# Kernel tuning notes

Hardware: AMD Instinct MI355X
Metric: run time of the kernel (lower is better)

Reference implementation:

```python
import jax, jax.numpy as jnp
import numpy as np

NODE_DIM = 256
EDGE_DIM = 128
HEADS = 8
HEAD_DIM = 32
HIDDEN = HEADS * HEAD_DIM  # 256
B, N = 2, 768
LN_EPS = 1e-5


def _layernorm(x, w, b):
    mu = jnp.mean(x, axis=-1, keepdims=True)
    var = jnp.mean(jnp.square(x - mu), axis=-1, keepdims=True)
    return (x - mu) * jax.lax.rsqrt(var + LN_EPS) * w + b


def setup_inputs() -> dict:
    key = jax.random.key(0)
    ks = jax.random.split(key, 10)
    s_node = NODE_DIM ** -0.5
    s_edge = EDGE_DIM ** -0.5
    s_hid = HIDDEN ** -0.5
    return {
        "node": jax.random.normal(ks[0], (B, N, NODE_DIM), jnp.float32),
        "edge": jax.random.normal(ks[1], (B, N, N, EDGE_DIM), jnp.float32),
        "ln_node_w": jnp.ones((NODE_DIM,), jnp.float32),
        "ln_node_b": jnp.zeros((NODE_DIM,), jnp.float32),
        "ln_edge_w": jnp.ones((EDGE_DIM,), jnp.float32),
        "ln_edge_b": jnp.zeros((EDGE_DIM,), jnp.float32),
        "Wq": jax.random.normal(ks[2], (NODE_DIM, HIDDEN), jnp.float32) * s_node,
        "Wk": jax.random.normal(ks[3], (NODE_DIM, HIDDEN), jnp.float32) * s_node,
        "Wv": jax.random.normal(ks[4], (NODE_DIM, HIDDEN), jnp.float32) * s_node,
        "Wb": jax.random.normal(ks[5], (EDGE_DIM, HEADS), jnp.float32) * s_edge,
        "Wg": jax.random.normal(ks[6], (NODE_DIM, HIDDEN), jnp.float32) * s_node,
        "bg": jnp.zeros((HIDDEN,), jnp.float32),
        "Wo": jax.random.normal(ks[7], (HIDDEN, NODE_DIM), jnp.float32) * s_hid,
        "bo": jnp.zeros((NODE_DIM,), jnp.float32),
    }


def reference(node, edge, ln_node_w, ln_node_b, ln_edge_w, ln_edge_b,
              Wq, Wk, Wv, Wb, Wg, bg, Wo, bo):
    scale = HEAD_DIM ** -0.5
    x = _layernorm(node, ln_node_w, ln_node_b)          # [b, i, node_dim]
    y = _layernorm(edge, ln_edge_w, ln_edge_b)          # [b, i, j, edge_dim]

    def heads(t):  # [b, i, hidden] -> [b, h, i, d]
        b_, i_, _ = t.shape
        return t.reshape(b_, i_, HEADS, HEAD_DIM).transpose(0, 2, 1, 3)

    q = heads(x @ Wq)
    k = heads(x @ Wk)
    v = heads(x @ Wv)
    g = heads(jax.nn.sigmoid(x @ Wg + bg))
    bias = jnp.einsum('bije,eh->bhij', y, Wb)           # [b, h, i, j]

    logits = jnp.einsum('bhid,bhjd->bhij', q, k) * scale + bias
    attn = jax.nn.softmax(logits, axis=-1)
    res = jnp.einsum('bhij,bhjd->bhid', attn, v) * g    # gated values
    res = res.transpose(0, 2, 1, 3).reshape(node.shape[0], node.shape[1], HIDDEN)
    return res @ Wo + bo
```

## Files before the change

### kernel.cpp

```cpp
#include <hip/hip_runtime.h>
#include <hip/hip_bf16.h>
#include <math.h>

#define BN 1536
#define NN 768
#define SCALE 0.17677669529663687f
#define NROWS (BN * NN)

__device__ __forceinline__ float sel8(const float* a, int idx) {
    float r = a[0];
#pragma unroll
    for (int t = 1; t < 8; ++t) r = (idx == t) ? a[t] : r;
    return r;
}

__global__ __launch_bounds__(256) void k_lnproj(
    const float* __restrict__ node, const float* __restrict__ lnw,
    const float* __restrict__ lnb, const float* __restrict__ Wq,
    const float* __restrict__ Wk, const float* __restrict__ Wv,
    const float* __restrict__ Wg, const float* __restrict__ bg,
    float* __restrict__ q, float* __restrict__ k,
    float* __restrict__ v, float* __restrict__ g)
{
    __shared__ float xs[8][256];
    const int tid = threadIdx.x;
    const int wave = tid >> 6, lane = tid & 63;
    const int row0 = blockIdx.x * 8;

#pragma unroll
    for (int rr = 0; rr < 2; ++rr) {
        const int r = wave * 2 + rr;
        float4 xv = ((const float4*)node)[(size_t)(row0 + r) * 64 + lane];
        float s1 = xv.x + xv.y + xv.z + xv.w;
        float s2 = fmaf(xv.x, xv.x, fmaf(xv.y, xv.y, fmaf(xv.z, xv.z, xv.w * xv.w)));
#pragma unroll
        for (int off = 32; off > 0; off >>= 1) {
            s1 += __shfl_xor(s1, off);
            s2 += __shfl_xor(s2, off);
        }
        const float mu = s1 * (1.f / 256.f);
        const float rstd = rsqrtf(s2 * (1.f / 256.f) - mu * mu + 1e-5f);
        float4 w4 = ((const float4*)lnw)[lane];
        float4 b4 = ((const float4*)lnb)[lane];
        xs[r][lane * 4 + 0] = (xv.x - mu) * rstd * w4.x + b4.x;
        xs[r][lane * 4 + 1] = (xv.y - mu) * rstd * w4.y + b4.y;
        xs[r][lane * 4 + 2] = (xv.z - mu) * rstd * w4.z + b4.z;
        xs[r][lane * 4 + 3] = (xv.w - mu) * rstd * w4.w + b4.w;
    }
    __syncthreads();

    float aq[8] = {}, ak[8] = {}, av[8] = {}, ag[8] = {};
    for (int e4 = 0; e4 < 64; ++e4) {
        const int e = e4 * 4;
        float wq_[4], wk_[4], wv_[4], wg_[4];
#pragma unroll
        for (int t = 0; t < 4; ++t) {
            wq_[t] = Wq[(e + t) * 256 + tid];
            wk_[t] = Wk[(e + t) * 256 + tid];
            wv_[t] = Wv[(e + t) * 256 + tid];
            wg_[t] = Wg[(e + t) * 256 + tid];
        }
#pragma unroll
        for (int r = 0; r < 8; ++r) {
            float4 xr = *(const float4*)&xs[r][e];
            aq[r] = fmaf(xr.x, wq_[0], fmaf(xr.y, wq_[1], fmaf(xr.z, wq_[2], fmaf(xr.w, wq_[3], aq[r]))));
            ak[r] = fmaf(xr.x, wk_[0], fmaf(xr.y, wk_[1], fmaf(xr.z, wk_[2], fmaf(xr.w, wk_[3], ak[r]))));
            av[r] = fmaf(xr.x, wv_[0], fmaf(xr.y, wv_[1], fmaf(xr.z, wv_[2], fmaf(xr.w, wv_[3], av[r]))));
            ag[r] = fmaf(xr.x, wg_[0], fmaf(xr.y, wg_[1], fmaf(xr.z, wg_[2], fmaf(xr.w, wg_[3], ag[r]))));
        }
    }
    const float bgv = bg[tid];
#pragma unroll
    for (int r = 0; r < 8; ++r) {
        const size_t o = (size_t)(row0 + r) * 256 + tid;
        q[o] = aq[r] * SCALE;
        k[o] = ak[r];
        v[o] = av[r];
        g[o] = 1.f / (1.f + __expf(-(ag[r] + bgv)));
    }
}

__global__ __launch_bounds__(256) void k_bias(
    const float* __restrict__ edge, const float* __restrict__ lnw,
    const float* __restrict__ lnb, const float* __restrict__ Wb,
    float* __restrict__ bias)
{
    const int tid = threadIdx.x;
    const int gl = tid & 15;

    float wbf[8][8];
    float c1p[8], c0p[8];
#pragma unroll
    for (int hh = 0; hh < 8; ++hh) { c1p[hh] = 0.f; c0p[hh] = 0.f; }
#pragma unroll
    for (int t = 0; t < 8; ++t) {
        const int c = gl * 8 + t;
        const float w = lnw[c], bb = lnb[c];
#pragma unroll
        for (int hh = 0; hh < 8; ++hh) {
            const float wb_ = Wb[c * 8 + hh];
            wbf[t][hh] = w * wb_;
            c1p[hh] += wbf[t][hh];
            c0p[hh] = fmaf(bb, wb_, c0p[hh]);
        }
    }
#pragma unroll
    for (int off = 1; off < 16; off <<= 1) {
#pragma unroll
        for (int hh = 0; hh < 8; ++hh) {
            c1p[hh] += __shfl_xor(c1p[hh], off);
            c0p[hh] += __shfl_xor(c0p[hh], off);
        }
    }
    const float c1s = sel8(c1p, gl & 7);
    const float c0s = sel8(c0p, gl & 7);

    const int stride = gridDim.x * 16;
    for (int r = blockIdx.x * 16 + (tid >> 4); r < NROWS; r += stride) {
        const float4 e0 = ((const float4*)edge)[(size_t)r * 32 + gl * 2];
        const float4 e1 = ((const float4*)edge)[(size_t)r * 32 + gl * 2 + 1];
        float s1 = (e0.x + e0.y) + (e0.z + e0.w) + ((e1.x + e1.y) + (e1.z + e1.w));
        float s2 = fmaf(e0.x, e0.x, fmaf(e0.y, e0.y, fmaf(e0.z, e0.z, e0.w * e0.w)));
        s2 = fmaf(e1.x, e1.x, fmaf(e1.y, e1.y, fmaf(e1.z, e1.z, fmaf(e1.w, e1.w, s2))));
        float d[8];
#pragma unroll
        for (int hh = 0; hh < 8; ++hh) {
            float t0 = e0.x * wbf[0][hh];
            t0 = fmaf(e0.y, wbf[1][hh], t0);
            t0 = fmaf(e0.z, wbf[2][hh], t0);
            t0 = fmaf(e0.w, wbf[3][hh], t0);
            t0 = fmaf(e1.x, wbf[4][hh], t0);
            t0 = fmaf(e1.y, wbf[5][hh], t0);
            t0 = fmaf(e1.z, wbf[6][hh], t0);
            t0 = fmaf(e1.w, wbf[7][hh], t0);
            d[hh] = t0;
        }
#pragma unroll
        for (int off = 1; off < 16; off <<= 1) {
            s1 += __shfl_xor(s1, off);
            s2 += __shfl_xor(s2, off);
#pragma unroll
            for (int hh = 0; hh < 8; ++hh) d[hh] += __shfl_xor(d[hh], off);
        }
        if (gl < 8) {
            const float mu = s1 * (1.f / 128.f);
            const float rstd = rsqrtf(s2 * (1.f / 128.f) - mu * mu + 1e-5f);
            const float dh = sel8(d, gl);
            bias[(size_t)r * 8 + gl] = rstd * (dh - mu * c1s) + c0s;
        }
    }
}

__global__ __launch_bounds__(256) void k_attn2(
    const float* __restrict__ bias,
    const float* __restrict__ q, const float* __restrict__ k,
    const float* __restrict__ v, const float* __restrict__ g,
    float* __restrict__ res)
{
    __shared__ float mrg[4][64][6];
    const int tid = threadIdx.x;
    const int wave = tid >> 6, lane = tid & 63;
    const int bi = blockIdx.x;
    const int b = bi / NN;
    const int h = lane >> 3;

    const float4 q4 = ((const float4*)q)[(size_t)bi * 64 + lane];
    const float* brow = bias + (size_t)bi * NN * 8;
    const size_t kb = (size_t)b * NN * 64;

    float m = -3e38f, s = 0.f;
    float4 acc = make_float4(0.f, 0.f, 0.f, 0.f);

    for (int jp = wave * 2; jp < NN; jp += 8) {
        const int j0 = jp, j1 = jp + 1;
        const float4 k0 = ((const float4*)k)[kb + (size_t)j0 * 64 + lane];
        const float4 k1 = ((const float4*)k)[kb + (size_t)j1 * 64 + lane];
        const float b0 = brow[j0 * 8 + h];
        const float b1 = brow[j1 * 8 + h];
        const float4 v0 = ((const float4*)v)[kb + (size_t)j0 * 64 + lane];
        const float4 v1 = ((const float4*)v)[kb + (size_t)j1 * 64 + lane];

        float d0 = fmaf(q4.x, k0.x, fmaf(q4.y, k0.y, fmaf(q4.z, k0.z, q4.w * k0.w)));
        float d1 = fmaf(q4.x, k1.x, fmaf(q4.y, k1.y, fmaf(q4.z, k1.z, q4.w * k1.w)));
        d0 += __shfl_xor(d0, 1); d1 += __shfl_xor(d1, 1);
        d0 += __shfl_xor(d0, 2); d1 += __shfl_xor(d1, 2);
        d0 += __shfl_xor(d0, 4); d1 += __shfl_xor(d1, 4);
        const float l0 = d0 + b0;
        const float l1 = d1 + b1;

        const float mn = fmaxf(m, fmaxf(l0, l1));
        const float sc = __expf(m - mn);
        const float p0 = __expf(l0 - mn);
        const float p1 = __expf(l1 - mn);
        s = fmaf(s, sc, p0 + p1);
        m = mn;
        acc.x = fmaf(p1, v1.x, fmaf(p0, v0.x, acc.x * sc));
        acc.y = fmaf(p1, v1.y, fmaf(p0, v0.y, acc.y * sc));
        acc.z = fmaf(p1, v1.z, fmaf(p0, v0.z, acc.z * sc));
        acc.w = fmaf(p1, v1.w, fmaf(p0, v0.w, acc.w * sc));
    }

    mrg[wave][lane][0] = m;
    mrg[wave][lane][1] = s;
    mrg[wave][lane][2] = acc.x;
    mrg[wave][lane][3] = acc.y;
    mrg[wave][lane][4] = acc.z;
    mrg[wave][lane][5] = acc.w;
    __syncthreads();
    if (wave == 0) {
        float M = mrg[0][lane][0];
#pragma unroll
        for (int w2 = 1; w2 < 4; ++w2) M = fmaxf(M, mrg[w2][lane][0]);
        float S = 0.f;
        float4 A = make_float4(0.f, 0.f, 0.f, 0.f);
#pragma unroll
        for (int w2 = 0; w2 < 4; ++w2) {
            const float sc = __expf(mrg[w2][lane][0] - M);
            S = fmaf(mrg[w2][lane][1], sc, S);
            A.x = fmaf(mrg[w2][lane][2], sc, A.x);
            A.y = fmaf(mrg[w2][lane][3], sc, A.y);
            A.z = fmaf(mrg[w2][lane][4], sc, A.z);
            A.w = fmaf(mrg[w2][lane][5], sc, A.w);
        }
        const float4 g4 = ((const float4*)g)[(size_t)bi * 64 + lane];
        const float inv = 1.f / S;
        float4 r;
        r.x = A.x * inv * g4.x;
        r.y = A.y * inv * g4.y;
        r.z = A.z * inv * g4.z;
        r.w = A.w * inv * g4.w;
        ((float4*)res)[(size_t)bi * 64 + lane] = r;
    }
}

__global__ __launch_bounds__(256) void k_outproj(
    const float* __restrict__ res, const float* __restrict__ Wo,
    const float* __restrict__ bo, float* __restrict__ out)
{
    __shared__ float xs[8][256];
    const int tid = threadIdx.x;
    const int row0 = blockIdx.x * 8;

#pragma unroll
    for (int t = tid; t < 512; t += 256)
        ((float4*)&xs[0][0])[t] = ((const float4*)(res + (size_t)row0 * 256))[t];
    __syncthreads();

    float a[8] = {};
    for (int e4 = 0; e4 < 64; ++e4) {
        const int e = e4 * 4;
        float w_[4];
#pragma unroll
        for (int t = 0; t < 4; ++t) w_[t] = Wo[(e + t) * 256 + tid];
#pragma unroll
        for (int r = 0; r < 8; ++r) {
            float4 xr = *(const float4*)&xs[r][e];
            a[r] = fmaf(xr.x, w_[0], fmaf(xr.y, w_[1], fmaf(xr.z, w_[2], fmaf(xr.w, w_[3], a[r]))));
        }
    }
    const float bov = bo[tid];
#pragma unroll
    for (int r = 0; r < 8; ++r)
        out[(size_t)(row0 + r) * 256 + tid] = a[r] + bov;
}

extern "C" void kernel_launch(void* const* d_in, const int* in_sizes, int n_in,
                              void* d_out, int out_size, void* d_ws, size_t ws_size,
                              hipStream_t stream) {
    const float* node = (const float*)d_in[0];
    const float* edge = (const float*)d_in[1];
    const float* lnnw = (const float*)d_in[2];
    const float* lnnb = (const float*)d_in[3];
    const float* lnew = (const float*)d_in[4];
    const float* lneb = (const float*)d_in[5];
    const float* Wq   = (const float*)d_in[6];
    const float* Wk   = (const float*)d_in[7];
    const float* Wv   = (const float*)d_in[8];
    const float* Wb   = (const float*)d_in[9];
    const float* Wg   = (const float*)d_in[10];
    const float* bg   = (const float*)d_in[11];
    const float* Wo   = (const float*)d_in[12];
    const float* bo   = (const float*)d_in[13];
    float* out = (float*)d_out;

    float* ws = (float*)d_ws;
    const size_t NT = (size_t)BN * 256;
    float* q    = ws;
    float* k    = ws + NT;
    float* v    = ws + 2 * NT;
    float* g    = ws + 3 * NT;
    float* res  = ws + 4 * NT;
    float* bias = ws + 5 * NT;

    k_lnproj<<<BN / 8, 256, 0, stream>>>(node, lnnw, lnnb, Wq, Wk, Wv, Wg, bg, q, k, v, g);
    k_bias<<<2048, 256, 0, stream>>>(edge, lnew, lneb, Wb, bias);
    k_attn2<<<BN, 256, 0, stream>>>(bias, q, k, v, g, res);
    k_outproj<<<BN / 8, 256, 0, stream>>>(res, Wo, bo, out);
}
```

Baseline: 405.3 us.

## Prefetch edge rows and K/V tiles, use DPP reductions, one query row per wave

The bias kernel now gives each wave a contiguous 288-row chunk, loads channel-interleaved float4s, software-prefetches the next rows, and replaces shuffle reductions with DPP row reductions. The attention kernel maps one query row per wave instead of splitting the keys across four waves, so the LDS merge and the barrier go away. It processes 4 keys per step with register double-buffered K/V and bias prefetch, using DPP for part of the dot-product reduction. The risks are fewer waves working on each row (1536 waves total), higher register pressure, and a longer serial loop per wave.

```diff
diff --git a/kernel.cpp b/kernel.cpp
--- a/kernel.cpp
+++ b/kernel.cpp
@@ -12,6 +12,27 @@
 #pragma unroll
     for (int t = 1; t < 8; ++t) r = (idx == t) ? a[t] : r;
     return r;
+}
+
+__device__ __forceinline__ float dpp_add16(float x) {
+    int t;
+    t = __builtin_amdgcn_update_dpp(0, __float_as_int(x), 0x128, 0xF, 0xF, true);
+    x += __int_as_float(t);
+    t = __builtin_amdgcn_update_dpp(0, __float_as_int(x), 0x124, 0xF, 0xF, true);
+    x += __int_as_float(t);
+    t = __builtin_amdgcn_update_dpp(0, __float_as_int(x), 0x122, 0xF, 0xF, true);
+    x += __int_as_float(t);
+    t = __builtin_amdgcn_update_dpp(0, __float_as_int(x), 0x121, 0xF, 0xF, true);
+    x += __int_as_float(t);
+    return x;
+}
+__device__ __forceinline__ float dpp_xor1_add(float x) {
+    int t = __builtin_amdgcn_update_dpp(0, __float_as_int(x), 0xB1, 0xF, 0xF, true);
+    return x + __int_as_float(t);
+}
+__device__ __forceinline__ float dpp_xor2_add(float x) {
+    int t = __builtin_amdgcn_update_dpp(0, __float_as_int(x), 0x4E, 0xF, 0xF, true);
+    return x + __int_as_float(t);
 }
 
 __global__ __launch_bounds__(256) void k_lnproj(
@@ -80,87 +101,107 @@
     }
 }
 
-__global__ __launch_bounds__(256) void k_bias(
+__global__ __launch_bounds__(256, 4) void k_bias(
     const float* __restrict__ edge, const float* __restrict__ lnw,
     const float* __restrict__ lnb, const float* __restrict__ Wb,
     float* __restrict__ bias)
 {
     const int tid = threadIdx.x;
-    const int gl = tid & 15;
+    const int wv = tid >> 6, lane = tid & 63;
+    const int gl = lane & 15;
+    const int rg = lane >> 4;
 
     float wbf[8][8];
-    float c1p[8], c0p[8];
-#pragma unroll
-    for (int hh = 0; hh < 8; ++hh) { c1p[hh] = 0.f; c0p[hh] = 0.f; }
+    float c1s[8], c0s[8];
+#pragma unroll
+    for (int hh = 0; hh < 8; ++hh) { c1s[hh] = 0.f; c0s[hh] = 0.f; }
 #pragma unroll
     for (int t = 0; t < 8; ++t) {
-        const int c = gl * 8 + t;
+        const int c = (t < 4) ? (gl * 4 + t) : (64 + gl * 4 + (t - 4));
         const float w = lnw[c], bb = lnb[c];
+        const float4 wa = ((const float4*)Wb)[c * 2];
+        const float4 wc = ((const float4*)Wb)[c * 2 + 1];
+        wbf[t][0] = w * wa.x; wbf[t][1] = w * wa.y;
+        wbf[t][2] = w * wa.z; wbf[t][3] = w * wa.w;
+        wbf[t][4] = w * wc.x; wbf[t][5] = w * wc.y;
+        wbf[t][6] = w * wc.z; wbf[t][7] = w * wc.w;
+        c0s[0] = fmaf(bb, wa.x, c0s[0]); c0s[1] = fmaf(bb, wa.y, c0s[1]);
+        c0s[2] = fmaf(bb, wa.z, c0s[2]); c0s[3] = fmaf(bb, wa.w, c0s[3]);
+        c0s[4] = fmaf(bb, wc.x, c0s[4]); c0s[5] = fmaf(bb, wc.y, c0s[5]);
+        c0s[6] = fmaf(bb, wc.z, c0s[6]); c0s[7] = fmaf(bb, wc.w, c0s[7]);
+#pragma unroll
+        for (int hh = 0; hh < 8; ++hh) c1s[hh] += wbf[t][hh];
+    }
+#pragma unroll
+    for (int hh = 0; hh < 8; ++hh) {
+        c1s[hh] = dpp_add16(c1s[hh]);
+        c0s[hh] = dpp_add16(c0s[hh]);
+    }
+    const float c1l = sel8(c1s, gl & 7);
+    const float c0l = sel8(c0s, gl & 7);
+
+    const int w = blockIdx.x * 4 + wv;
+    const int row0 = w * 288;
+    const float4* ep = (const float4*)edge;
+
+    float4 a0, a1, b0, b1;
+    {
+        const size_t r = (size_t)(row0 + rg);
+        a0 = ep[r * 32 + gl];
+        a1 = ep[r * 32 + 16 + gl];
+    }
+
+    for (int it = 0; it < 72; ++it) {
+        if (it < 71) {
+            const size_t r = (size_t)(row0 + (it + 1) * 4 + rg);
+            b0 = ep[r * 32 + gl];
+            b1 = ep[r * 32 + 16 + gl];
+        }
+
+        float s1 = ((a0.x + a0.y) + (a0.z + a0.w)) + ((a1.x + a1.y) + (a1.z + a1.w));
+        float s2 = fmaf(a0.x, a0.x, fmaf(a0.y, a0.y, fmaf(a0.z, a0.z, a0.w * a0.w)));
+        s2 = fmaf(a1.x, a1.x, fmaf(a1.y, a1.y, fmaf(a1.z, a1.z, fmaf(a1.w, a1.w, s2))));
+
+        float d[8];
 #pragma unroll
         for (int hh = 0; hh < 8; ++hh) {
-            const float wb_ = Wb[c * 8 + hh];
-            wbf[t][hh] = w * wb_;
-            c1p[hh] += wbf[t][hh];
-            c0p[hh] = fmaf(bb, wb_, c0p[hh]);
-        }
-    }
-#pragma unroll
-    for (int off = 1; off < 16; off <<= 1) {
-#pragma unroll
-        for (int hh = 0; hh < 8; ++hh) {
-            c1p[hh] += __shfl_xor(c1p[hh], off);
-            c0p[hh] += __shfl_xor(c0p[hh], off);
-        }
-    }
-    const float c1s = sel8(c1p, gl & 7);
-    const float c0s = sel8(c0p, gl & 7);
-
-    const int stride = gridDim.x * 16;
-    for (int r = blockIdx.x * 16 + (tid >> 4); r < NROWS; r += stride) {
-        const float4 e0 = ((const float4*)edge)[(size_t)r * 32 + gl * 2];
-        const float4 e1 = ((const float4*)edge)[(size_t)r * 32 + gl * 2 + 1];
-        float s1 = (e0.x + e0.y) + (e0.z + e0.w) + ((e1.x + e1.y) + (e1.z + e1.w));
-        float s2 = fmaf(e0.x, e0.x, fmaf(e0.y, e0.y, fmaf(e0.z, e0.z, e0.w * e0.w)));
-        s2 = fmaf(e1.x, e1.x, fmaf(e1.y, e1.y, fmaf(e1.z, e1.z, fmaf(e1.w, e1.w, s2))));
-        float d[8];
-#pragma unroll
-        for (int hh = 0; hh < 8; ++hh) {
-            float t0 = e0.x * wbf[0][hh];
-            t0 = fmaf(e0.y, wbf[1][hh], t0);
-            t0 = fmaf(e0.z, wbf[2][hh], t0);
-            t0 = fmaf(e0.w, wbf[3][hh], t0);
-            t0 = fmaf(e1.x, wbf[4][hh], t0);
-            t0 = fmaf(e1.y, wbf[5][hh], t0);
-            t0 = fmaf(e1.z, wbf[6][hh], t0);
-            t0 = fmaf(e1.w, wbf[7][hh], t0);
-            d[hh] = t0;
-        }
-#pragma unroll
-        for (int off = 1; off < 16; off <<= 1) {
-            s1 += __shfl_xor(s1, off);
-            s2 += __shfl_xor(s2, off);
-#pragma unroll
-            for (int hh = 0; hh < 8; ++hh) d[hh] += __shfl_xor(d[hh], off);
-        }
+            float a = a0.x * wbf[0][hh];
+            a = fmaf(a0.y, wbf[1][hh], a);
+            a = fmaf(a0.z, wbf[2][hh], a);
+            a = fmaf(a0.w, wbf[3][hh], a);
+            a = fmaf(a1.x, wbf[4][hh], a);
+            a = fmaf(a1.y, wbf[5][hh], a);
+            a = fmaf(a1.z, wbf[6][hh], a);
+            a = fmaf(a1.w, wbf[7][hh], a);
+            d[hh] = a;
+        }
+
+        s1 = dpp_add16(s1);
+        s2 = dpp_add16(s2);
+#pragma unroll
+        for (int hh = 0; hh < 8; ++hh) d[hh] = dpp_add16(d[hh]);
+
+        const float mu = s1 * (1.f / 128.f);
+        const float rstd = rsqrtf(s2 * (1.f / 128.f) - mu * mu + 1e-5f);
         if (gl < 8) {
-            const float mu = s1 * (1.f / 128.f);
-            const float rstd = rsqrtf(s2 * (1.f / 128.f) - mu * mu + 1e-5f);
             const float dh = sel8(d, gl);
-            bias[(size_t)r * 8 + gl] = rstd * (dh - mu * c1s) + c0s;
-        }
-    }
-}
-
-__global__ __launch_bounds__(256) void k_attn2(
+            bias[(size_t)(row0 + it * 4 + rg) * 8 + gl] =
+                rstd * (dh - mu * c1l) + c0l;
+        }
+
+        a0 = b0; a1 = b1;
+    }
+}
+
+__global__ __launch_bounds__(256) void k_attn4(
     const float* __restrict__ bias,
     const float* __restrict__ q, const float* __restrict__ k,
     const float* __restrict__ v, const float* __restrict__ g,
     float* __restrict__ res)
 {
-    __shared__ float mrg[4][64][6];
     const int tid = threadIdx.x;
-    const int wave = tid >> 6, lane = tid & 63;
-    const int bi = blockIdx.x;
+    const int wv = tid >> 6, lane = tid & 63;
+    const int bi = blockIdx.x * 4 + wv;
     const int b = bi / NN;
     const int h = lane >> 3;
 
@@ -171,66 +212,79 @@
     float m = -3e38f, s = 0.f;
     float4 acc = make_float4(0.f, 0.f, 0.f, 0.f);
 
-    for (int jp = wave * 2; jp < NN; jp += 8) {
-        const int j0 = jp, j1 = jp + 1;
-        const float4 k0 = ((const float4*)k)[kb + (size_t)j0 * 64 + lane];
-        const float4 k1 = ((const float4*)k)[kb + (size_t)j1 * 64 + lane];
-        const float b0 = brow[j0 * 8 + h];
-        const float b1 = brow[j1 * 8 + h];
-        const float4 v0 = ((const float4*)v)[kb + (size_t)j0 * 64 + lane];
-        const float4 v1 = ((const float4*)v)[kb + (size_t)j1 * 64 + lane];
-
-        float d0 = fmaf(q4.x, k0.x, fmaf(q4.y, k0.y, fmaf(q4.z, k0.z, q4.w * k0.w)));
-        float d1 = fmaf(q4.x, k1.x, fmaf(q4.y, k1.y, fmaf(q4.z, k1.z, q4.w * k1.w)));
-        d0 += __shfl_xor(d0, 1); d1 += __shfl_xor(d1, 1);
-        d0 += __shfl_xor(d0, 2); d1 += __shfl_xor(d1, 2);
-        d0 += __shfl_xor(d0, 4); d1 += __shfl_xor(d1, 4);
-        const float l0 = d0 + b0;
-        const float l1 = d1 + b1;
-
-        const float mn = fmaxf(m, fmaxf(l0, l1));
+    float4 kc[4], vc[4];
+    float bc[4], bn1[4];
+#pragma unroll
+    for (int u = 0; u < 4; ++u) {
+        kc[u] = ((const float4*)k)[kb + (size_t)u * 64 + lane];
+        vc[u] = ((const float4*)v)[kb + (size_t)u * 64 + lane];
+        bc[u]  = brow[u * 8 + h];
+        bn1[u] = brow[(4 + u) * 8 + h];
+    }
+
+    for (int t = 0; t < NN / 4; ++t) {
+        float4 kn[4], vn[4];
+        float bn2[4];
+        if (t + 2 < NN / 4) {
+#pragma unroll
+            for (int u = 0; u < 4; ++u)
+                bn2[u] = brow[((t + 2) * 4 + u) * 8 + h];
+        }
+        if (t + 1 < NN / 4) {
+#pragma unroll
+            for (int u = 0; u < 4; ++u) {
+                kn[u] = ((const float4*)k)[kb + (size_t)((t + 1) * 4 + u) * 64 + lane];
+                vn[u] = ((const float4*)v)[kb + (size_t)((t + 1) * 4 + u) * 64 + lane];
+            }
+        }
+
+        float l[4];
+#pragma unroll
+        for (int u = 0; u < 4; ++u) {
+            float d = fmaf(q4.x, kc[u].x, fmaf(q4.y, kc[u].y,
+                      fmaf(q4.z, kc[u].z, q4.w * kc[u].w)));
+            d = dpp_xor1_add(d);
+            d = dpp_xor2_add(d);
+            d += __shfl_xor(d, 4);
+            l[u] = d + bc[u];
+        }
+        const float lm = fmaxf(fmaxf(l[0], l[1]), fmaxf(l[2], l[3]));
+        const float mn = fmaxf(m, lm);
         const float sc = __expf(m - mn);
-        const float p0 = __expf(l0 - mn);
-        const float p1 = __expf(l1 - mn);
-        s = fmaf(s, sc, p0 + p1);
+        float p[4];
+#pragma unroll
+        for (int u = 0; u < 4; ++u) p[u] = __expf(l[u] - mn);
+        s = fmaf(s, sc, (p[0] + p[1]) + (p[2] + p[3]));
         m = mn;
-        acc.x = fmaf(p1, v1.x, fmaf(p0, v0.x, acc.x * sc));
-        acc.y = fmaf(p1, v1.y, fmaf(p0, v0.y, acc.y * sc));
-        acc.z = fmaf(p1, v1.z, fmaf(p0, v0.z, acc.z * sc));
-        acc.w = fmaf(p1, v1.w, fmaf(p0, v0.w, acc.w * sc));
-    }
-
-    mrg[wave][lane][0] = m;
-    mrg[wave][lane][1] = s;
-    mrg[wave][lane][2] = acc.x;
-    mrg[wave][lane][3] = acc.y;
-    mrg[wave][lane][4] = acc.z;
-    mrg[wave][lane][5] = acc.w;
-    __syncthreads();
-    if (wave == 0) {
-        float M = mrg[0][lane][0];
-#pragma unroll
-        for (int w2 = 1; w2 < 4; ++w2) M = fmaxf(M, mrg[w2][lane][0]);
-        float S = 0.f;
-        float4 A = make_float4(0.f, 0.f, 0.f, 0.f);
-#pragma unroll
-        for (int w2 = 0; w2 < 4; ++w2) {
-            const float sc = __expf(mrg[w2][lane][0] - M);
-            S = fmaf(mrg[w2][lane][1], sc, S);
-            A.x = fmaf(mrg[w2][lane][2], sc, A.x);
-            A.y = fmaf(mrg[w2][lane][3], sc, A.y);
-            A.z = fmaf(mrg[w2][lane][4], sc, A.z);
-            A.w = fmaf(mrg[w2][lane][5], sc, A.w);
-        }
-        const float4 g4 = ((const float4*)g)[(size_t)bi * 64 + lane];
-        const float inv = 1.f / S;
-        float4 r;
-        r.x = A.x * inv * g4.x;
-        r.y = A.y * inv * g4.y;
-        r.z = A.z * inv * g4.z;
-        r.w = A.w * inv * g4.w;
-        ((float4*)res)[(size_t)bi * 64 + lane] = r;
-    }
+        acc.x = fmaf(p[3], vc[3].x, fmaf(p[2], vc[2].x,
+                fmaf(p[1], vc[1].x, fmaf(p[0], vc[0].x, acc.x * sc))));
+        acc.y = fmaf(p[3], vc[3].y, fmaf(p[2], vc[2].y,
+                fmaf(p[1], vc[1].y, fmaf(p[0], vc[0].y, acc.y * sc))));
+        acc.z = fmaf(p[3], vc[3].z, fmaf(p[2], vc[2].z,
+                fmaf(p[1], vc[1].z, fmaf(p[0], vc[0].z, acc.z * sc))));
+        acc.w = fmaf(p[3], vc[3].w, fmaf(p[2], vc[2].w,
+                fmaf(p[1], vc[1].w, fmaf(p[0], vc[0].w, acc.w * sc))));
+
+        if (t + 1 < NN / 4) {
+#pragma unroll
+            for (int u = 0; u < 4; ++u) { kc[u] = kn[u]; vc[u] = vn[u]; }
+        }
+#pragma unroll
+        for (int u = 0; u < 4; ++u) bc[u] = bn1[u];
+        if (t + 2 < NN / 4) {
+#pragma unroll
+            for (int u = 0; u < 4; ++u) bn1[u] = bn2[u];
+        }
+    }
+
+    const float4 g4 = ((const float4*)g)[(size_t)bi * 64 + lane];
+    const float inv = 1.f / s;
+    float4 r;
+    r.x = acc.x * inv * g4.x;
+    r.y = acc.y * inv * g4.y;
+    r.z = acc.z * inv * g4.z;
+    r.w = acc.w * inv * g4.w;
+    ((float4*)res)[(size_t)bi * 64 + lane] = r;
 }
 
 __global__ __launch_bounds__(256) void k_outproj(
@@ -293,7 +347,7 @@
     float* bias = ws + 5 * NT;
 
     k_lnproj<<<BN / 8, 256, 0, stream>>>(node, lnnw, lnnb, Wq, Wk, Wv, Wg, bg, q, k, v, g);
-    k_bias<<<2048, 256, 0, stream>>>(edge, lnew, lneb, Wb, bias);
-    k_attn2<<<BN, 256, 0, stream>>>(bias, q, k, v, g, res);
+    k_bias<<<1024, 256, 0, stream>>>(edge, lnew, lneb, Wb, bias);
+    k_attn4<<<BN / 4, 256, 0, stream>>>(bias, q, k, v, g, res);
     k_outproj<<<BN / 8, 256, 0, stream>>>(res, Wo, bo, out);
 }
```

Measured after the change: 353.8 us. -12.7%, faster.
